# Performance work log

Hardware: AMD Instinct MI355X
Metric: run time of the kernel (lower is better)

Reference implementation:

```python
import jax, jax.numpy as jnp
import numpy as np
import math

EMBED_DIM = 512
VOCAB = 96          # 95 printable ASCII + <UNK>
N_TOKENS = 16384
ALPHA = 1.5
BETA = 0.8
FRACTAL = 1.7
THETA = 0.1          # SO(4) rotation angle
LN_EPS = 1e-5        # torch LayerNorm default


def _semantic_table():
    """Faithful per-character semantic weights, L2-normalized rows. [VOCAB,4]."""
    wmap = {
        'vowels': [1.2, 0.8, 1.5, 0.9],
        'consonants': [0.9, 1.1, 0.7, 1.3],
        'digits': [1.0, 1.0, 1.0, 1.0],
        'punctuation': [0.5, 0.5, 0.8, 0.8],
        'whitespace': [0.3, 0.3, 0.3, 0.3],
        'unknown': [0.1, 0.1, 0.1, 0.1],
    }
    vocab = [chr(i) for i in range(32, 127)] + ['<UNK>']

    def cat(c):
        if c in 'aeiouAEIOU':
            return 'vowels'
        if c in 'bcdfghjklmnpqrstvwxyzBCDFGHJKLMNPQRSTVWXYZ':
            return 'consonants'
        if c in '0123456789':
            return 'digits'
        if c == ' ':
            return 'whitespace'
        if c == '<UNK>':
            return 'unknown'
        return 'punctuation'

    t = np.array([wmap[cat(c)] for c in vocab], dtype=np.float32)
    return t / np.linalg.norm(t, axis=1, keepdims=True)


def setup_inputs() -> dict:
    key = jax.random.key(0)
    k1, k2, k3, k4 = jax.random.split(key, 4)
    D, N = EMBED_DIM, N_TOKENS
    return {
        'char_idx': jax.random.randint(k1, (N,), 0, VOCAB, dtype=jnp.int32),
        'positions': jax.random.randint(k2, (N,), 0, 512, dtype=jnp.int32),
        'W': jax.random.normal(k3, (D, D), dtype=jnp.float32) * (1.0 / math.sqrt(D)),
        'b': jnp.zeros((D,), dtype=jnp.float32),
        'gamma': jnp.ones((D,), dtype=jnp.float32),
        'beta_ln': jnp.zeros((D,), dtype=jnp.float32),
        'noise': jax.random.normal(k4, (N, D), dtype=jnp.float32),  # scaled by 0.01 inside
        'sem_table': jnp.asarray(_semantic_table()),
    }


def reference(char_idx, positions, W, b, gamma, beta_ln, noise, sem_table):
    D = EMBED_DIM
    lam = char_idx.astype(jnp.float32) / VOCAB          # [N]
    t = positions.astype(jnp.float32) / 100.0           # [N]
    omega = 2.0 * math.pi * ALPHA
    kwav = 2.0 * math.pi / FRACTAL

    # Padilha wave equation (per-token complex scalars)
    ph1 = omega * t - kwav * lam + BETA * lam ** 2
    ph2 = omega * t * 1.5 - kwav * lam * 0.7 + BETA * lam ** 2 * 1.3
    a1 = jnp.sin(omega * t + ALPHA * lam)
    a2 = jnp.cos(omega * t * 0.8 + ALPHA * lam * 1.2)
    wf1 = a1 * jnp.exp(1j * ph1)                         # [N] complex64
    wf2 = a2 * jnp.exp(1j * ph2)

    i = jnp.arange(D, dtype=jnp.float32)                 # [D]
    mod1 = jnp.exp(1j * (2.0 * math.pi / D) * i[None, :] * lam[:, None])          # [N,D]
    mod2 = jnp.exp(1j * (4.0 * math.pi / D) * 1.7 * i[None, :] * lam[:, None])
    w1 = 0.6 + 0.4 * jnp.sin(0.1 * i)
    w2 = 0.4 + 0.6 * jnp.cos(0.15 * i)
    state = w1 * wf1[:, None] * mod1 + w2 * wf2[:, None] * mod2                   # [N,D] complex

    # Spectral filtering + per-token L2 normalization
    kv = jnp.arange(1, D + 1, dtype=jnp.float32)
    filt = (0.7 * jnp.exp(1j * ALPHA * jnp.arctan(jnp.log(kv + 1e-10)))
            + 0.3 * jnp.exp(1j * BETA * jnp.sin(0.1 * kv)))
    state = state * filt
    nrm = jnp.sqrt(jnp.sum(jnp.abs(state) ** 2, axis=-1, keepdims=True))
    state = state / (nrm + 1e-8)

    # SO(4) rotation, then take real part
    ct, st = math.cos(THETA), math.sin(THETA)
    x = state.real * ct - state.imag * st                # [N,D] float32

    # Adaptive linear + LayerNorm + noise
    x = x @ W.T + b
    mu = jnp.mean(x, axis=-1, keepdims=True)
    var = jnp.mean((x - mu) ** 2, axis=-1, keepdims=True)
    y = (x - mu) / jnp.sqrt(var + LN_EPS) * gamma + beta_ln + 0.01 * noise

    # Quaternion embedding
    sw = sem_table[char_idx]                             # [N,4]
    phase = (2.0 * math.pi / D) * jnp.arange(D, dtype=jnp.float32)  # [D]
    cpm = char_idx.astype(jnp.float32) * 0.01            # [N]
    q1 = y * sw[:, 0:1] * jnp.cos(phase[None, :] + cpm[:, None])
    q2 = y * sw[:, 1:2] * jnp.sin(phase[None, :] + cpm[:, None] * 1.3)
    q3 = y * sw[:, 2:3] * jnp.cos(2.0 * phase[None, :] + cpm[:, None] * 0.7)
    return jnp.stack([y, q1, q2, q3], axis=-1)           # [N,D,4]
```

## Files before the change

kernel.cpp:

```cpp
#include <hip/hip_runtime.h>
#include <math.h>

#define N_TOK 16384
#define D_DIM 512
#define PI_F 3.14159265358979323846f

typedef __bf16 bf16x8 __attribute__((ext_vector_type(8)));
typedef __bf16 bf16x4 __attribute__((ext_vector_type(4)));
typedef float floatx4 __attribute__((ext_vector_type(4)));

__global__ __launch_bounds__(256) void setup_kernel(
    const float* __restrict__ W, float4* __restrict__ table,
    __bf16* __restrict__ Wb) {
  const int bid = blockIdx.x;
  const int tid = threadIdx.x;
  if (bid < 96) {
    const float lam = (float)bid / 96.0f;
#pragma unroll
    for (int q = 0; q < 2; ++q) {
      const int d = tid + q * 256;
      const float fi = (float)d;
      float s1, c1, s2, c2;
      sincosf((2.0f * PI_F / 512.0f) * fi * lam, &s1, &c1);
      sincosf((4.0f * PI_F / 512.0f) * 1.7f * fi * lam, &s2, &c2);
      const float w1 = 0.6f + 0.4f * sinf(0.1f * fi);
      const float w2 = 0.4f + 0.6f * cosf(0.15f * fi);
      const float kv = fi + 1.0f;
      float fs1, fc1, fs2, fc2;
      sincosf(1.5f * atanf(logf(kv + 1e-10f)), &fs1, &fc1);
      sincosf(0.8f * sinf(0.1f * kv), &fs2, &fc2);
      const float fre = 0.7f * fc1 + 0.3f * fc2;
      const float fim = 0.7f * fs1 + 0.3f * fs2;
      table[bid * 512 + d] = make_float4(
          w1 * (c1 * fre - s1 * fim), w1 * (c1 * fim + s1 * fre),
          w2 * (c2 * fre - s2 * fim), w2 * (c2 * fim + s2 * fre));
    }
  } else {
    const int i = (bid - 96) * 256 + tid;
    const float4 w = ((const float4*)W)[i];
    bf16x4 o;
    o[0] = (__bf16)w.x; o[1] = (__bf16)w.y; o[2] = (__bf16)w.z; o[3] = (__bf16)w.w;
    ((bf16x4*)Wb)[i] = o;
  }
}

__global__ __launch_bounds__(256) void fused_kernel(
    const int* __restrict__ char_idx, const int* __restrict__ pos,
    const float4* __restrict__ table, const __bf16* __restrict__ Wb,
    const float* __restrict__ b, const float* __restrict__ gamma,
    const float* __restrict__ beta_ln, const float* __restrict__ noise,
    const float* __restrict__ sem, float4* __restrict__ out) {
  __shared__ __align__(16) __bf16 A_lds[16 * 2 * 64 * 8];
  __shared__ float2 rc1[32], rc2[32], rc3[32];
  __shared__ float part[4][32][2];
  __shared__ float stats[32][2];

  const int tid = threadIdx.x;
  const int lane = tid & 63, w = tid >> 6;
  const int row0 = blockIdx.x * 32;
  const float ct = 0.99500416527f, st = 0.09983341664f;

  for (int rr = 0; rr < 8; ++rr) {
    const int m = w * 8 + rr;
    const int n = row0 + m;
    const int c = char_idx[n];
    const float lam = (float)c * (1.0f / 96.0f);
    const float t = (float)pos[n] * 0.01f;
    const float omega = 2.0f * PI_F * 1.5f;
    const float kwav = 2.0f * PI_F / 1.7f;
    const float lam2 = lam * lam;
    float sp1, cp1, sp2, cp2;
    __sincosf(omega * t - kwav * lam + 0.8f * lam2, &sp1, &cp1);
    __sincosf(omega * t * 1.5f - kwav * lam * 0.7f + 1.04f * lam2, &sp2, &cp2);
    const float a1 = __sinf(omega * t + 1.5f * lam);
    const float a2 = __cosf(omega * t * 0.8f + 1.8f * lam);
    const float w1re = a1 * cp1, w1im = a1 * sp1;
    const float w2re = a2 * cp2, w2im = a2 * sp2;

    const float4* tp = table + c * 512 + lane * 8;
    float zre[8], zim[8], ss = 0.0f;
#pragma unroll
    for (int j = 0; j < 8; ++j) {
      const float4 mm = tp[j];
      zre[j] = w1re * mm.x - w1im * mm.y + w2re * mm.z - w2im * mm.w;
      zim[j] = w1re * mm.y + w1im * mm.x + w2re * mm.w + w2im * mm.z;
      ss += zre[j] * zre[j] + zim[j] * zim[j];
    }
#pragma unroll
    for (int off = 32; off > 0; off >>= 1) ss += __shfl_down(ss, off, 64);
    ss = __shfl(ss, 0, 64);
    const float inv = 1.0f / (sqrtf(ss) + 1e-8f);
    bf16x8 av;
#pragma unroll
    for (int j = 0; j < 8; ++j) av[j] = (__bf16)((zre[j] * ct - zim[j] * st) * inv);
    const int kc = lane >> 2, prt = lane & 3, mt = m >> 4;
    *(bf16x8*)(A_lds + (((kc * 2 + mt) * 64) + ((prt << 4) | (m & 15))) * 8) = av;

    if (lane == 0) {
      const float cpm = (float)c * 0.01f;
      float s, cc;
      __sincosf(cpm, &s, &cc);
      rc1[m] = make_float2(sem[c * 4 + 0] * cc, sem[c * 4 + 0] * s);
      __sincosf(cpm * 1.3f, &s, &cc);
      rc2[m] = make_float2(sem[c * 4 + 1] * cc, sem[c * 4 + 1] * s);
      __sincosf(cpm * 0.7f, &s, &cc);
      rc3[m] = make_float2(sem[c * 4 + 2] * cc, sem[c * 4 + 2] * s);
    }
  }
  __syncthreads();

  const int cl = lane & 15, kq = lane >> 4;
  const int wn = w * 128;
  const __bf16* Bbase = Wb + (size_t)(wn + cl) * 512 + kq * 8;
  floatx4 acc[2][8] = {};
  bf16x8 bcur[8], bnxt[8];
#pragma unroll
  for (int j = 0; j < 8; ++j) bcur[j] = *(const bf16x8*)(Bbase + j * 16 * 512);
  for (int kc = 0; kc < 16; ++kc) {
    if (kc < 15) {
#pragma unroll
      for (int j = 0; j < 8; ++j)
        bnxt[j] = *(const bf16x8*)(Bbase + j * 16 * 512 + (kc + 1) * 32);
    }
    const bf16x8 a0 = *(const bf16x8*)(A_lds + ((kc * 2 + 0) * 64 + lane) * 8);
    const bf16x8 a1 = *(const bf16x8*)(A_lds + ((kc * 2 + 1) * 64 + lane) * 8);
#pragma unroll
    for (int j = 0; j < 8; ++j) {
      acc[0][j] = __builtin_amdgcn_mfma_f32_16x16x32_bf16(a0, bcur[j], acc[0][j], 0, 0, 0);
      acc[1][j] = __builtin_amdgcn_mfma_f32_16x16x32_bf16(a1, bcur[j], acc[1][j], 0, 0, 0);
    }
#pragma unroll
    for (int j = 0; j < 8; ++j) bcur[j] = bnxt[j];
  }

  float bj[8], gj[8], btj[8], cph[8], sph[8];
#pragma unroll
  for (int j = 0; j < 8; ++j) {
    const int col = wn + j * 16 + cl;
    bj[j] = b[col]; gj[j] = gamma[col]; btj[j] = beta_ln[col];
    __sincosf((2.0f * PI_F / 512.0f) * (float)col, &sph[j], &cph[j]);
  }
  float ps[8] = {}, ps2[8] = {};
#pragma unroll
  for (int i = 0; i < 2; ++i)
#pragma unroll
    for (int j = 0; j < 8; ++j)
#pragma unroll
      for (int r = 0; r < 4; ++r) {
        const float v = acc[i][j][r] + bj[j];
        acc[i][j][r] = v;
        ps[i * 4 + r] += v;
        ps2[i * 4 + r] += v * v;
      }
#pragma unroll
  for (int mask = 1; mask < 16; mask <<= 1)
#pragma unroll
    for (int tt = 0; tt < 8; ++tt) {
      ps[tt] += __shfl_xor(ps[tt], mask, 64);
      ps2[tt] += __shfl_xor(ps2[tt], mask, 64);
    }
  if (cl == 0) {
#pragma unroll
    for (int i = 0; i < 2; ++i)
#pragma unroll
      for (int r = 0; r < 4; ++r) {
        const int m = i * 16 + kq * 4 + r;
        part[w][m][0] = ps[i * 4 + r];
        part[w][m][1] = ps2[i * 4 + r];
      }
  }
  __syncthreads();
  if (tid < 32) {
    const float s = part[0][tid][0] + part[1][tid][0] + part[2][tid][0] + part[3][tid][0];
    const float s2 = part[0][tid][1] + part[1][tid][1] + part[2][tid][1] + part[3][tid][1];
    const float mu = s * (1.0f / 512.0f);
    const float var = s2 * (1.0f / 512.0f) - mu * mu;
    stats[tid][0] = mu;
    stats[tid][1] = rsqrtf(var + 1e-5f);
  }
  __syncthreads();

#pragma unroll
  for (int i = 0; i < 2; ++i)
#pragma unroll
    for (int r = 0; r < 4; ++r) {
      const int m = i * 16 + kq * 4 + r;
      const float mu = stats[m][0], rstd = stats[m][1];
      const float2 c1 = rc1[m], c2 = rc2[m], c3 = rc3[m];
      const size_t rowoff = (size_t)(row0 + m) * 512;
#pragma unroll
      for (int j = 0; j < 8; ++j) {
        const int col = wn + j * 16 + cl;
        const float y = (acc[i][j][r] - mu) * rstd * gj[j] + btj[j]
                        + 0.01f * noise[rowoff + col];
        const float c2p = cph[j] * cph[j] - sph[j] * sph[j];
        const float s2p = 2.0f * sph[j] * cph[j];
        const float q1 = y * (c1.x * cph[j] - c1.y * sph[j]);
        const float q2 = y * (c2.x * sph[j] + c2.y * cph[j]);
        const float q3 = y * (c3.x * c2p - c3.y * s2p);
        out[rowoff + col] = make_float4(y, q1, q2, q3);
      }
    }
}

extern "C" void kernel_launch(void* const* d_in, const int* in_sizes, int n_in,
                              void* d_out, int out_size, void* d_ws, size_t ws_size,
                              hipStream_t stream) {
  const int* char_idx = (const int*)d_in[0];
  const int* pos      = (const int*)d_in[1];
  const float* W      = (const float*)d_in[2];
  const float* b      = (const float*)d_in[3];
  const float* gamma  = (const float*)d_in[4];
  const float* beta_ln= (const float*)d_in[5];
  const float* noise  = (const float*)d_in[6];
  const float* sem    = (const float*)d_in[7];

  float4* table = (float4*)d_ws;
  __bf16* Wb    = (__bf16*)(table + 96 * 512);

  setup_kernel<<<352, 256, 0, stream>>>(W, table, Wb);
  fused_kernel<<<N_TOK / 32, 256, 0, stream>>>(char_idx, pos, table, Wb, b,
                                               gamma, beta_ln, noise, sem,
                                               (float4*)d_out);
}
```

Measured before the change: 247.3 us.

## Pre-swizzle W into MFMA fragment layout and use 512-thread blocks

The setup kernel now writes W as bf16 in the exact per-lane MFMA B-fragment order, so each lane's B loads are contiguous and coalesced. The fused kernel moves to 8 waves per block, each covering 64 output columns instead of 128, which halves per-wave accumulators and B registers and raises occupancy (launch bounds 512,4). A-fragment LDS reads are also prefetched one k-step ahead, and the norm reduction uses xor shuffles. The cost is more waves sharing the same A tile and more LayerNorm partials to combine.

```diff
diff --git a/kernel.cpp b/kernel.cpp
--- a/kernel.cpp
+++ b/kernel.cpp
@@ -2,16 +2,14 @@
 #include <math.h>
 
 #define N_TOK 16384
-#define D_DIM 512
 #define PI_F 3.14159265358979323846f
 
 typedef __bf16 bf16x8 __attribute__((ext_vector_type(8)));
-typedef __bf16 bf16x4 __attribute__((ext_vector_type(4)));
 typedef float floatx4 __attribute__((ext_vector_type(4)));
 
 __global__ __launch_bounds__(256) void setup_kernel(
     const float* __restrict__ W, float4* __restrict__ table,
-    __bf16* __restrict__ Wb) {
+    __bf16* __restrict__ Bf) {
   const int bid = blockIdx.x;
   const int tid = threadIdx.x;
   if (bid < 96) {
@@ -37,31 +35,36 @@
     }
   } else {
     const int i = (bid - 96) * 256 + tid;
-    const float4 w = ((const float4*)W)[i];
-    bf16x4 o;
-    o[0] = (__bf16)w.x; o[1] = (__bf16)w.y; o[2] = (__bf16)w.z; o[3] = (__bf16)w.w;
-    ((bf16x4*)Wb)[i] = o;
+    const int ct = i >> 10;
+    const int kc = (i >> 6) & 15;
+    const int lane = i & 63;
+    const int cl = lane & 15, kq = lane >> 4;
+    const float* src = W + (size_t)(ct * 16 + cl) * 512 + kc * 32 + kq * 8;
+    bf16x8 o;
+#pragma unroll
+    for (int j = 0; j < 8; ++j) o[j] = (__bf16)src[j];
+    *(bf16x8*)(Bf + (size_t)i * 8) = o;
   }
 }
 
-__global__ __launch_bounds__(256) void fused_kernel(
+__global__ __launch_bounds__(512, 4) void fused_kernel(
     const int* __restrict__ char_idx, const int* __restrict__ pos,
-    const float4* __restrict__ table, const __bf16* __restrict__ Wb,
+    const float4* __restrict__ table, const __bf16* __restrict__ Bf,
     const float* __restrict__ b, const float* __restrict__ gamma,
     const float* __restrict__ beta_ln, const float* __restrict__ noise,
     const float* __restrict__ sem, float4* __restrict__ out) {
   __shared__ __align__(16) __bf16 A_lds[16 * 2 * 64 * 8];
   __shared__ float2 rc1[32], rc2[32], rc3[32];
-  __shared__ float part[4][32][2];
+  __shared__ float part[8][32][2];
   __shared__ float stats[32][2];
 
   const int tid = threadIdx.x;
   const int lane = tid & 63, w = tid >> 6;
   const int row0 = blockIdx.x * 32;
-  const float ct = 0.99500416527f, st = 0.09983341664f;
-
-  for (int rr = 0; rr < 8; ++rr) {
-    const int m = w * 8 + rr;
+  const float ctR = 0.99500416527f, stR = 0.09983341664f;
+
+  for (int rr = 0; rr < 4; ++rr) {
+    const int m = w * 4 + rr;
     const int n = row0 + m;
     const int c = char_idx[n];
     const float lam = (float)c * (1.0f / 96.0f);
@@ -87,12 +90,11 @@
       ss += zre[j] * zre[j] + zim[j] * zim[j];
     }
 #pragma unroll
-    for (int off = 32; off > 0; off >>= 1) ss += __shfl_down(ss, off, 64);
-    ss = __shfl(ss, 0, 64);
+    for (int off = 32; off > 0; off >>= 1) ss += __shfl_xor(ss, off, 64);
     const float inv = 1.0f / (sqrtf(ss) + 1e-8f);
     bf16x8 av;
 #pragma unroll
-    for (int j = 0; j < 8; ++j) av[j] = (__bf16)((zre[j] * ct - zim[j] * st) * inv);
+    for (int j = 0; j < 8; ++j) av[j] = (__bf16)((zre[j] * ctR - zim[j] * stR) * inv);
     const int kc = lane >> 2, prt = lane & 3, mt = m >> 4;
     *(bf16x8*)(A_lds + (((kc * 2 + mt) * 64) + ((prt << 4) | (m & 15))) * 8) = av;
 
@@ -110,33 +112,36 @@
   __syncthreads();
 
   const int cl = lane & 15, kq = lane >> 4;
-  const int wn = w * 128;
-  const __bf16* Bbase = Wb + (size_t)(wn + cl) * 512 + kq * 8;
-  floatx4 acc[2][8] = {};
-  bf16x8 bcur[8], bnxt[8];
-#pragma unroll
-  for (int j = 0; j < 8; ++j) bcur[j] = *(const bf16x8*)(Bbase + j * 16 * 512);
+  const __bf16* Bp = Bf + ((size_t)(w * 4) * 16 + 0) * 64 * 8 + lane * 8;
+  floatx4 acc[2][4] = {};
+  bf16x8 bcur[4], bnxt[4];
+  bf16x8 a0 = *(const bf16x8*)(A_lds + lane * 8);
+  bf16x8 a1 = *(const bf16x8*)(A_lds + (64 + lane) * 8);
+  bf16x8 a0n, a1n;
+#pragma unroll
+  for (int j = 0; j < 4; ++j) bcur[j] = *(const bf16x8*)(Bp + (size_t)(j * 16) * 512);
   for (int kc = 0; kc < 16; ++kc) {
     if (kc < 15) {
 #pragma unroll
-      for (int j = 0; j < 8; ++j)
-        bnxt[j] = *(const bf16x8*)(Bbase + j * 16 * 512 + (kc + 1) * 32);
-    }
-    const bf16x8 a0 = *(const bf16x8*)(A_lds + ((kc * 2 + 0) * 64 + lane) * 8);
-    const bf16x8 a1 = *(const bf16x8*)(A_lds + ((kc * 2 + 1) * 64 + lane) * 8);
-#pragma unroll
-    for (int j = 0; j < 8; ++j) {
+      for (int j = 0; j < 4; ++j)
+        bnxt[j] = *(const bf16x8*)(Bp + (size_t)(j * 16 + kc + 1) * 512);
+      a0n = *(const bf16x8*)(A_lds + (((kc + 1) * 2 + 0) * 64 + lane) * 8);
+      a1n = *(const bf16x8*)(A_lds + (((kc + 1) * 2 + 1) * 64 + lane) * 8);
+    }
+#pragma unroll
+    for (int j = 0; j < 4; ++j) {
       acc[0][j] = __builtin_amdgcn_mfma_f32_16x16x32_bf16(a0, bcur[j], acc[0][j], 0, 0, 0);
       acc[1][j] = __builtin_amdgcn_mfma_f32_16x16x32_bf16(a1, bcur[j], acc[1][j], 0, 0, 0);
     }
-#pragma unroll
-    for (int j = 0; j < 8; ++j) bcur[j] = bnxt[j];
-  }
-
-  float bj[8], gj[8], btj[8], cph[8], sph[8];
-#pragma unroll
-  for (int j = 0; j < 8; ++j) {
-    const int col = wn + j * 16 + cl;
+    a0 = a0n; a1 = a1n;
+#pragma unroll
+    for (int j = 0; j < 4; ++j) bcur[j] = bnxt[j];
+  }
+
+  float bj[4], gj[4], btj[4], cph[4], sph[4];
+#pragma unroll
+  for (int j = 0; j < 4; ++j) {
+    const int col = w * 64 + j * 16 + cl;
     bj[j] = b[col]; gj[j] = gamma[col]; btj[j] = beta_ln[col];
     __sincosf((2.0f * PI_F / 512.0f) * (float)col, &sph[j], &cph[j]);
   }
@@ -144,7 +149,7 @@
 #pragma unroll
   for (int i = 0; i < 2; ++i)
 #pragma unroll
-    for (int j = 0; j < 8; ++j)
+    for (int j = 0; j < 4; ++j)
 #pragma unroll
       for (int r = 0; r < 4; ++r) {
         const float v = acc[i][j][r] + bj[j];
@@ -171,8 +176,9 @@
   }
   __syncthreads();
   if (tid < 32) {
-    const float s = part[0][tid][0] + part[1][tid][0] + part[2][tid][0] + part[3][tid][0];
-    const float s2 = part[0][tid][1] + part[1][tid][1] + part[2][tid][1] + part[3][tid][1];
+    float s = 0.0f, s2 = 0.0f;
+#pragma unroll
+    for (int ww = 0; ww < 8; ++ww) { s += part[ww][tid][0]; s2 += part[ww][tid][1]; }
     const float mu = s * (1.0f / 512.0f);
     const float var = s2 * (1.0f / 512.0f) - mu * mu;
     stats[tid][0] = mu;
@@ -189,8 +195,8 @@
       const float2 c1 = rc1[m], c2 = rc2[m], c3 = rc3[m];
       const size_t rowoff = (size_t)(row0 + m) * 512;
 #pragma unroll
-      for (int j = 0; j < 8; ++j) {
-        const int col = wn + j * 16 + cl;
+      for (int j = 0; j < 4; ++j) {
+        const int col = w * 64 + j * 16 + cl;
         const float y = (acc[i][j][r] - mu) * rstd * gj[j] + btj[j]
                         + 0.01f * noise[rowoff + col];
         const float c2p = cph[j] * cph[j] - sph[j] * sph[j];
@@ -216,10 +222,10 @@
   const float* sem    = (const float*)d_in[7];
 
   float4* table = (float4*)d_ws;
-  __bf16* Wb    = (__bf16*)(table + 96 * 512);
-
-  setup_kernel<<<352, 256, 0, stream>>>(W, table, Wb);
-  fused_kernel<<<N_TOK / 32, 256, 0, stream>>>(char_idx, pos, table, Wb, b,
+  __bf16* Bf    = (__bf16*)(table + 96 * 512);
+
+  setup_kernel<<<224, 256, 0, stream>>>(W, table, Bf);
+  fused_kernel<<<N_TOK / 32, 512, 0, stream>>>(char_idx, pos, table, Bf, b,
                                                gamma, beta_ln, noise, sem,
                                                (float4*)d_out);
 }
```

After: 206.4 us. 1.2x faster.
